# Kernel tuning notes

Hardware: AMD Instinct MI355X
Metric: run time of the kernel (lower is better)

## Reference

```python
import jax, jax.numpy as jnp
import numpy as np

B, N, C_IN, C_OUT = 4, 2048, 1024, 1024


def setup_inputs() -> dict:
    key = jax.random.key(0)
    ks = jax.random.split(key, 4)
    scale = 1.0 / np.sqrt(C_IN)
    return {
        "hidden_states": jax.random.normal(ks[0], (B, N, C_IN), dtype=jnp.float32),
        "Wq": jax.random.normal(ks[1], (C_OUT, C_IN), dtype=jnp.float32) * scale,
        "bq": jnp.zeros((C_OUT,), dtype=jnp.float32),
        "Wk": jax.random.normal(ks[2], (C_OUT, C_IN), dtype=jnp.float32) * scale,
        "bk": jnp.zeros((C_OUT,), dtype=jnp.float32),
        "Wv": jax.random.normal(ks[3], (C_OUT, C_IN), dtype=jnp.float32) * scale,
        "bv": jnp.zeros((C_OUT,), dtype=jnp.float32),
    }


def reference(hidden_states, Wq, bq, Wk, bk, Wv, bv):
    # torch nn.Linear: y = x @ W.T + b
    Q = jnp.einsum("bnc,dc->bnd", hidden_states, Wq) + bq
    K = jnp.einsum("bnc,dc->bnd", hidden_states, Wk) + bk
    V = jnp.einsum("bnc,dc->bnd", hidden_states, Wv) + bv
    d_k = K.shape[-1]
    scores = jnp.einsum("bnd,bmd->bnm", Q, K) * (d_k ** -0.5)  # [B,N,N]
    attention = jax.nn.softmax(scores, axis=-1)
    out = jnp.einsum("bnm,bmd->bnd", attention, V)
    return (out, attention)
```

## Files before the change

### kernel.cpp

```cpp
#include <hip/hip_runtime.h>
#include <cstdint>

typedef __attribute__((ext_vector_type(8))) short bf16x8;
typedef __attribute__((ext_vector_type(4))) float f32x4;

__device__ __forceinline__ unsigned short f2bf(float v) {
  unsigned u = __builtin_bit_cast(unsigned, v);
  u += 0x7FFFu + ((u >> 16) & 1u);
  return (unsigned short)(u >> 16);
}

__device__ __forceinline__ void gload16(const unsigned short* g, unsigned short* l) {
  __builtin_amdgcn_global_load_lds(
      (const __attribute__((address_space(1))) void*)(uintptr_t)g,
      (__attribute__((address_space(3))) void*)(uint32_t)(uintptr_t)l,
      16, 0, 0);
}

__device__ __forceinline__ bf16x8 ds_read128(const unsigned short* p) {
  bf16x8 r;
  asm volatile("ds_read_b128 %0, %1"
               : "=v"(r)
               : "v"((uint32_t)(uintptr_t)p));
  return r;
}

#define BAR()   asm volatile("s_barrier" ::: "memory")
#define LGKM0() do { asm volatile("s_waitcnt lgkmcnt(0)" ::: "memory"); \
                     __builtin_amdgcn_sched_barrier(0); } while (0)
#define VMW(N)  asm volatile("s_waitcnt vmcnt(" #N ")" ::: "memory")

__device__ __forceinline__ void gemm_core(
    const unsigned short* __restrict__ A, const unsigned short* __restrict__ B,
    int lda, int ldb, int NT,
    unsigned short* lds, f32x4 acc[8][4])
{
  const int tid  = threadIdx.x;
  const int w    = tid >> 6;
  const int lane = tid & 63;
  const int wr   = w >> 2;
  const int wc   = w & 3;
  const int lrow = lane & 15;
  const int kq   = lane >> 4;

  const int srow = tid >> 3;
  const int schk = ((tid & 7) ^ (srow & 7)) * 8;
  const unsigned short* gA = A + (long)srow * lda + schk;
  const unsigned short* gB = B + (long)srow * ldb + schk;
  unsigned short* const stg = lds + w * 512;

  const int pc0 = ((0 + kq) ^ (lrow & 7)) * 8;
  const int pc1 = ((4 + kq) ^ (lrow & 7)) * 8;

  #define STG(g, ld, H, t, s) do { \
    gload16((g) + (long)(H)      * (ld) + (t) * 64, stg + (s) * 8192); \
    gload16((g) + (long)((H)+64) * (ld) + (t) * 64, stg + (s) * 8192 + 4096); \
  } while (0)

  STG(gB, ldb, 0,   0, 0);
  STG(gB, ldb, 128, 0, 1);
  STG(gA, lda, 0,   0, 2);
  STG(gA, lda, 128, 0, 3);
  STG(gB, ldb, 0,   1, 4);
  STG(gB, ldb, 128, 1, 5);
  VMW(4);
  BAR();

  for (int t = 0; t < NT; ++t) {
    const int base = (t & 1) * 32768;
    const unsigned short* lA = lds + base + (2 + wr) * 8192 + lrow * 64;
    const unsigned short* lB = lds + base + (wc >> 1) * 8192 + ((wc & 1) * 64 + lrow) * 64;
    const bool doA = (t + 1 < NT);
    const bool doB = (t + 2 < NT);

    bf16x8 bfr[4][2], af[2][2];
#pragma unroll
    for (int p = 0; p < 4; ++p) {
      if (p == 0) {
#pragma unroll
        for (int j = 0; j < 4; ++j) {
          bfr[j][0] = ds_read128(lB + j * 1024 + pc0);
          bfr[j][1] = ds_read128(lB + j * 1024 + pc1);
        }
      }
#pragma unroll
      for (int i = 0; i < 2; ++i) {
        af[i][0] = ds_read128(lA + (2 * p + i) * 1024 + pc0);
        af[i][1] = ds_read128(lA + (2 * p + i) * 1024 + pc1);
      }
      if (p == 0 && doA) STG(gA, lda, 0,   t + 1, ((t + 1) & 1) * 4 + 2);
      if (p == 1 && doA) STG(gA, lda, 128, t + 1, ((t + 1) & 1) * 4 + 3);
      if (p == 2 && doB) STG(gB, ldb, 0,   t + 2, (t & 1) * 4 + 0);
      if (p == 3 && doB) STG(gB, ldb, 128, t + 2, (t & 1) * 4 + 1);
      BAR();
      LGKM0();
      __builtin_amdgcn_s_setprio(1);
#pragma unroll
      for (int i = 0; i < 2; ++i)
#pragma unroll
        for (int j = 0; j < 4; ++j) {
          acc[2 * p + i][j] = __builtin_amdgcn_mfma_f32_16x16x32_bf16(af[i][0], bfr[j][0], acc[2 * p + i][j], 0, 0, 0);
          acc[2 * p + i][j] = __builtin_amdgcn_mfma_f32_16x16x32_bf16(af[i][1], bfr[j][1], acc[2 * p + i][j], 0, 0, 0);
        }
      __builtin_amdgcn_s_setprio(0);
      if (p == 3) {
        if (t < NT - 2)       { VMW(4); }
        else if (t == NT - 2) { VMW(0); }
      }
      BAR();
    }
  }
  #undef STG
}

__global__ __launch_bounds__(512, 2) void gemm_qkv(
    const unsigned short* __restrict__ xh,
    const unsigned short* __restrict__ wh,
    const float* __restrict__ bq, const float* __restrict__ bk, const float* __restrict__ bv,
    unsigned short* __restrict__ Qh, unsigned short* __restrict__ Kh,
    unsigned short* __restrict__ Vth)
{
  __shared__ __align__(16) unsigned short lds[65536];
  const int Mblk = blockIdx.x * 256;
  const int sel  = blockIdx.y >> 2;
  const int nb   = blockIdx.y & 3;

  const unsigned short* A = xh + (long)Mblk * 1024;
  const unsigned short* B = wh + sel * 1048576 + (long)(nb * 256) * 1024;
  const float* bias = (sel == 0) ? bq : (sel == 1) ? bk : bv;

  f32x4 acc[8][4] = {};
  gemm_core(A, B, 1024, 1024, 16, lds, acc);

  const int lane = threadIdx.x & 63, w = threadIdx.x >> 6;
  const int wr = w >> 2, wc = w & 3;
  const int lrow = lane & 15, kq = lane >> 4;

#pragma unroll
  for (int i = 0; i < 8; ++i) {
#pragma unroll
    for (int j = 0; j < 4; ++j) {
      const int col = nb * 256 + wc * 64 + j * 16 + lrow;
      const float bsv = bias[col];
#pragma unroll
      for (int r = 0; r < 4; ++r) {
        const int tok = Mblk + wr * 128 + i * 16 + kq * 4 + r;
        const unsigned short h = f2bf(acc[i][j][r] + bsv);
        if (sel == 2) {
          Vth[(long)(tok >> 11) * 2097152 + (long)col * 2048 + (tok & 2047)] = h;
        } else if (sel == 0) {
          Qh[(long)tok * 1024 + col] = h;
        } else {
          Kh[(long)tok * 1024 + col] = h;
        }
      }
    }
  }
}

__global__ __launch_bounds__(512, 2) void gemm_f32out(
    const unsigned short* __restrict__ A, const unsigned short* __restrict__ B,
    int lda, int ldb, int NT,
    long sA, long sB, float* __restrict__ C, int ldc, long sC, float alpha)
{
  __shared__ __align__(16) unsigned short lds[65536];
  const int Mblk = blockIdx.x * 256;
  const int Nblk = blockIdx.y * 256;
  const long z = blockIdx.z;
  const unsigned short* Ab = A + z * sA + (long)Mblk * lda;
  const unsigned short* Bb = B + z * sB + (long)Nblk * ldb;
  float* Cb = C + z * sC;

  f32x4 acc[8][4] = {};
  gemm_core(Ab, Bb, lda, ldb, NT, lds, acc);

  const int lane = threadIdx.x & 63, w = threadIdx.x >> 6;
  const int wr = w >> 2, wc = w & 3;
  const int lrow = lane & 15, kq = lane >> 4;
#pragma unroll
  for (int i = 0; i < 8; ++i)
#pragma unroll
    for (int j = 0; j < 4; ++j)
#pragma unroll
      for (int r = 0; r < 4; ++r) {
        const int row = Mblk + wr * 128 + i * 16 + kq * 4 + r;
        const int col = Nblk + wc * 64 + j * 16 + lrow;
        Cb[(long)row * ldc + col] = alpha * acc[i][j][r];
      }
}

__global__ __launch_bounds__(256) void softmax_rows(
    float* __restrict__ S, unsigned short* __restrict__ Ph)
{
  __shared__ float red[4];
  const long row = blockIdx.x;
  float* rp = S + row * 2048;
  const int t = threadIdx.x;

  float x[8];
  *(float4*)&x[0] = reinterpret_cast<const float4*>(rp)[t];
  *(float4*)&x[4] = reinterpret_cast<const float4*>(rp)[t + 256];

  float m = x[0];
#pragma unroll
  for (int i = 1; i < 8; ++i) m = fmaxf(m, x[i]);
  for (int o = 32; o; o >>= 1) m = fmaxf(m, __shfl_xor(m, o, 64));
  if ((t & 63) == 0) red[t >> 6] = m;
  __syncthreads();
  m = fmaxf(fmaxf(red[0], red[1]), fmaxf(red[2], red[3]));
  __syncthreads();

  float s = 0.f;
#pragma unroll
  for (int i = 0; i < 8; ++i) { x[i] = expf(x[i] - m); s += x[i]; }
  for (int o = 32; o; o >>= 1) s += __shfl_xor(s, o, 64);
  if ((t & 63) == 0) red[t >> 6] = s;
  __syncthreads();
  s = (red[0] + red[1]) + (red[2] + red[3]);
  const float inv = 1.0f / s;

#pragma unroll
  for (int i = 0; i < 8; ++i) x[i] *= inv;
  reinterpret_cast<float4*>(rp)[t]       = *(float4*)&x[0];
  reinterpret_cast<float4*>(rp)[t + 256] = *(float4*)&x[4];

  const long b0 = row * 2048 + t * 4;
#pragma unroll
  for (int k = 0; k < 4; ++k) Ph[b0 + k] = f2bf(x[k]);
  const long b1 = row * 2048 + 1024 + t * 4;
#pragma unroll
  for (int k = 0; k < 4; ++k) Ph[b1 + k] = f2bf(x[4 + k]);
}

__global__ __launch_bounds__(256) void to_bf16(
    const float* __restrict__ x, unsigned short* __restrict__ hi, int n4)
{
  int i = blockIdx.x * 256 + threadIdx.x;
  const int stride = gridDim.x * 256;
  for (; i < n4; i += stride) {
    const float4 v = reinterpret_cast<const float4*>(x)[i];
    ushort4 h;
    h.x = f2bf(v.x); h.y = f2bf(v.y); h.z = f2bf(v.z); h.w = f2bf(v.w);
    reinterpret_cast<ushort4*>(hi)[i] = h;
  }
}

extern "C" void kernel_launch(void* const* d_in, const int* in_sizes, int n_in,
                              void* d_out, int out_size, void* d_ws, size_t ws_size,
                              hipStream_t stream)
{
  const float* x  = (const float*)d_in[0];
  const float* Wq = (const float*)d_in[1];
  const float* bq = (const float*)d_in[2];
  const float* Wk = (const float*)d_in[3];
  const float* bk = (const float*)d_in[4];
  const float* Wv = (const float*)d_in[5];
  const float* bv = (const float*)d_in[6];

  float* out  = (float*)d_out;
  float* attn = (float*)d_out + 8388608;

  unsigned short* ws  = (unsigned short*)d_ws;
  unsigned short* xh  = ws;
  unsigned short* wh  = xh + 8388608;
  unsigned short* Qh  = wh + 3145728;
  unsigned short* Kh  = Qh + 8388608;
  unsigned short* Vth = Kh + 8388608;
  unsigned short* Ph  = Vth + 8388608;

  to_bf16<<<2048, 256, 0, stream>>>(x, xh, 2097152);
  to_bf16<<<512, 256, 0, stream>>>(Wq, wh, 262144);
  to_bf16<<<512, 256, 0, stream>>>(Wk, wh + 1048576, 262144);
  to_bf16<<<512, 256, 0, stream>>>(Wv, wh + 2097152, 262144);

  gemm_qkv<<<dim3(32, 12), 512, 0, stream>>>(xh, wh, bq, bk, bv, Qh, Kh, Vth);

  gemm_f32out<<<dim3(8, 8, 4), 512, 0, stream>>>(Qh, Kh, 1024, 1024, 16,
      2097152L, 2097152L, attn, 2048, 4194304L, 0.03125f);

  softmax_rows<<<8192, 256, 0, stream>>>(attn, Ph);

  gemm_f32out<<<dim3(8, 4, 4), 512, 0, stream>>>(Ph, Vth, 2048, 2048, 32,
      4194304L, 2097152L, out, 1024, 2097152L, 1.0f);
}
```

Baseline: 351.8 us.

## Software-pipeline LDS fragment reads in GEMM core and merge bf16 conversion launches

```diff
diff --git a/kernel.cpp b/kernel.cpp
--- a/kernel.cpp
+++ b/kernel.cpp
@@ -25,10 +25,10 @@
   return r;
 }
 
-#define BAR()   asm volatile("s_barrier" ::: "memory")
-#define LGKM0() do { asm volatile("s_waitcnt lgkmcnt(0)" ::: "memory"); \
-                     __builtin_amdgcn_sched_barrier(0); } while (0)
-#define VMW(N)  asm volatile("s_waitcnt vmcnt(" #N ")" ::: "memory")
+#define BAR()    asm volatile("s_barrier" ::: "memory")
+#define LGKMW(N) do { asm volatile("s_waitcnt lgkmcnt(" #N ")" ::: "memory"); \
+                      __builtin_amdgcn_sched_barrier(0); } while (0)
+#define VMW(N)   asm volatile("s_waitcnt vmcnt(" #N ")" ::: "memory")
 
 __device__ __forceinline__ void gemm_core(
     const unsigned short* __restrict__ A, const unsigned short* __restrict__ B,
@@ -66,48 +66,75 @@
   VMW(4);
   BAR();
 
+  bf16x8 afc[2][2], afn[2][2], bc[4][2], bn[4][2];
+  {
+    const unsigned short* lA0 = lds + (2 + wr) * 8192 + lrow * 64;
+    const unsigned short* lB0 = lds + (wc >> 1) * 8192 + ((wc & 1) * 64 + lrow) * 64;
+#pragma unroll
+    for (int j = 0; j < 4; ++j) {
+      bc[j][0] = ds_read128(lB0 + j * 1024 + pc0);
+      bc[j][1] = ds_read128(lB0 + j * 1024 + pc1);
+    }
+#pragma unroll
+    for (int i = 0; i < 2; ++i) {
+      afc[i][0] = ds_read128(lA0 + i * 1024 + pc0);
+      afc[i][1] = ds_read128(lA0 + i * 1024 + pc1);
+    }
+  }
+
   for (int t = 0; t < NT; ++t) {
-    const int base = (t & 1) * 32768;
-    const unsigned short* lA = lds + base + (2 + wr) * 8192 + lrow * 64;
-    const unsigned short* lB = lds + base + (wc >> 1) * 8192 + ((wc & 1) * 64 + lrow) * 64;
-    const bool doA = (t + 1 < NT);
-    const bool doB = (t + 2 < NT);
-
-    bf16x8 bfr[4][2], af[2][2];
+    const unsigned short* lA  = lds + (t & 1) * 32768 + (2 + wr) * 8192 + lrow * 64;
+    const unsigned short* lAn = lds + ((t + 1) & 1) * 32768 + (2 + wr) * 8192 + lrow * 64;
+    const unsigned short* lBn = lds + ((t + 1) & 1) * 32768 + (wc >> 1) * 8192 + ((wc & 1) * 64 + lrow) * 64;
+    const bool doA  = (t + 1 < NT);
+    const bool doB  = (t + 2 < NT);
+    const bool last = (t == NT - 1);
+
 #pragma unroll
     for (int p = 0; p < 4; ++p) {
-      if (p == 0) {
+      if (p < 3) {
+#pragma unroll
+        for (int i = 0; i < 2; ++i) {
+          afn[i][0] = ds_read128(lA + (2 * (p + 1) + i) * 1024 + pc0);
+          afn[i][1] = ds_read128(lA + (2 * (p + 1) + i) * 1024 + pc1);
+        }
+      } else if (!last) {
+        if (t == NT - 2) { VMW(0); } else { VMW(2); }
+#pragma unroll
+        for (int i = 0; i < 2; ++i) {
+          afn[i][0] = ds_read128(lAn + i * 1024 + pc0);
+          afn[i][1] = ds_read128(lAn + i * 1024 + pc1);
+        }
 #pragma unroll
         for (int j = 0; j < 4; ++j) {
-          bfr[j][0] = ds_read128(lB + j * 1024 + pc0);
-          bfr[j][1] = ds_read128(lB + j * 1024 + pc1);
-        }
-      }
-#pragma unroll
-      for (int i = 0; i < 2; ++i) {
-        af[i][0] = ds_read128(lA + (2 * p + i) * 1024 + pc0);
-        af[i][1] = ds_read128(lA + (2 * p + i) * 1024 + pc1);
+          bn[j][0] = ds_read128(lBn + j * 1024 + pc0);
+          bn[j][1] = ds_read128(lBn + j * 1024 + pc1);
+        }
       }
       if (p == 0 && doA) STG(gA, lda, 0,   t + 1, ((t + 1) & 1) * 4 + 2);
       if (p == 1 && doA) STG(gA, lda, 128, t + 1, ((t + 1) & 1) * 4 + 3);
       if (p == 2 && doB) STG(gB, ldb, 0,   t + 2, (t & 1) * 4 + 0);
       if (p == 3 && doB) STG(gB, ldb, 128, t + 2, (t & 1) * 4 + 1);
       BAR();
-      LGKM0();
+      if (p == 3) { if (last) { LGKMW(0); } else { LGKMW(12); } }
+      else       { LGKMW(4); }
       __builtin_amdgcn_s_setprio(1);
 #pragma unroll
       for (int i = 0; i < 2; ++i)
 #pragma unroll
         for (int j = 0; j < 4; ++j) {
-          acc[2 * p + i][j] = __builtin_amdgcn_mfma_f32_16x16x32_bf16(af[i][0], bfr[j][0], acc[2 * p + i][j], 0, 0, 0);
-          acc[2 * p + i][j] = __builtin_amdgcn_mfma_f32_16x16x32_bf16(af[i][1], bfr[j][1], acc[2 * p + i][j], 0, 0, 0);
+          acc[2 * p + i][j] = __builtin_amdgcn_mfma_f32_16x16x32_bf16(afc[i][0], bc[j][0], acc[2 * p + i][j], 0, 0, 0);
+          acc[2 * p + i][j] = __builtin_amdgcn_mfma_f32_16x16x32_bf16(afc[i][1], bc[j][1], acc[2 * p + i][j], 0, 0, 0);
         }
       __builtin_amdgcn_s_setprio(0);
-      if (p == 3) {
-        if (t < NT - 2)       { VMW(4); }
-        else if (t == NT - 2) { VMW(0); }
-      }
-      BAR();
+      if (p < 3 || !last) {
+#pragma unroll
+        for (int i = 0; i < 2; ++i) { afc[i][0] = afn[i][0]; afc[i][1] = afn[i][1]; }
+      }
+      if (p == 3 && !last) {
+#pragma unroll
+        for (int j = 0; j < 4; ++j) { bc[j][0] = bn[j][0]; bc[j][1] = bn[j][1]; }
+      }
     }
   }
   #undef STG
@@ -232,16 +259,27 @@
   for (int k = 0; k < 4; ++k) Ph[b1 + k] = f2bf(x[4 + k]);
 }
 
-__global__ __launch_bounds__(256) void to_bf16(
-    const float* __restrict__ x, unsigned short* __restrict__ hi, int n4)
-{
-  int i = blockIdx.x * 256 + threadIdx.x;
+__global__ __launch_bounds__(256) void to_bf16_all(
+    const float* __restrict__ x,
+    const float* __restrict__ Wq, const float* __restrict__ Wk,
+    const float* __restrict__ Wv,
+    unsigned short* __restrict__ xh, unsigned short* __restrict__ wh)
+{
   const int stride = gridDim.x * 256;
-  for (; i < n4; i += stride) {
-    const float4 v = reinterpret_cast<const float4*>(x)[i];
+  for (int i = blockIdx.x * 256 + threadIdx.x; i < 2883584; i += stride) {
+    const float* src; unsigned short* dst; int off;
+    if (i < 2097152)      { src = x;  dst = xh; off = i; }
+    else {
+      const int j = i - 2097152;
+      const int sel = j >> 18;
+      off = j & 262143;
+      src = (sel == 0) ? Wq : (sel == 1) ? Wk : Wv;
+      dst = wh + (long)sel * 1048576;
+    }
+    const float4 v = reinterpret_cast<const float4*>(src)[off];
     ushort4 h;
     h.x = f2bf(v.x); h.y = f2bf(v.y); h.z = f2bf(v.z); h.w = f2bf(v.w);
-    reinterpret_cast<ushort4*>(hi)[i] = h;
+    reinterpret_cast<ushort4*>(dst)[off] = h;
   }
 }
 
@@ -268,10 +306,7 @@
   unsigned short* Vth = Kh + 8388608;
   unsigned short* Ph  = Vth + 8388608;
 
-  to_bf16<<<2048, 256, 0, stream>>>(x, xh, 2097152);
-  to_bf16<<<512, 256, 0, stream>>>(Wq, wh, 262144);
-  to_bf16<<<512, 256, 0, stream>>>(Wk, wh + 1048576, 262144);
-  to_bf16<<<512, 256, 0, stream>>>(Wv, wh + 2097152, 262144);
+  to_bf16_all<<<2048, 256, 0, stream>>>(x, Wq, Wk, Wv, xh, wh);
 
   gemm_qkv<<<dim3(32, 12), 512, 0, stream>>>(xh, wh, bq, bk, bv, Qh, Kh, Vth);
 
```

After: 389.7 us. +10.8%, slower.
